# Performance work log

Measured on AMD Instinct MI355X. Metric: run time of the kernel, lower is better.

The kernel has to match this reference:

```python
import jax, jax.numpy as jnp
import numpy as np

NUM_GROUPS = 32
EPS = 1e-5


def group_norm(x, scale, bias):
    # x: [B, C, H, W]
    B, C, H, W = x.shape
    g = x.reshape(B, NUM_GROUPS, C // NUM_GROUPS * H * W)
    mean = g.mean(axis=-1, keepdims=True)
    var = g.var(axis=-1, keepdims=True)
    g = (g - mean) * jax.lax.rsqrt(var + EPS)
    g = g.reshape(B, C, H, W)
    return g * scale[None, :, None, None] + bias[None, :, None, None]


def conv1x1(x, w, b):
    # x: [B, C, H, W], w: [O, C], b: [O]
    return jnp.einsum('bchw,oc->bohw', x, w) + b[None, :, None, None]


def setup_inputs() -> dict:
    key = jax.random.key(0)
    ks = jax.random.split(key, 11)
    B, C, H, W = 32, 256, 32, 32
    s = 1.0 / np.sqrt(C)
    return {
        'x': jax.random.normal(ks[0], (B, C, H, W), jnp.float32),
        'gn_scale': jnp.ones((C,), jnp.float32),
        'gn_bias': jnp.zeros((C,), jnp.float32),
        'wq': jax.random.normal(ks[1], (C, C), jnp.float32) * s,
        'bq': jnp.zeros((C,), jnp.float32),
        'wk': jax.random.normal(ks[2], (C, C), jnp.float32) * s,
        'bk': jnp.zeros((C,), jnp.float32),
        'wv': jax.random.normal(ks[3], (C, C), jnp.float32) * s,
        'bv': jnp.zeros((C,), jnp.float32),
        'wo': jax.random.normal(ks[4], (C, C), jnp.float32) * s,
        'bo': jnp.zeros((C,), jnp.float32),
    }


def reference(x, gn_scale, gn_bias, wq, bq, wk, bk, wv, bv, wo, bo):
    B, C, H, W = x.shape
    h = group_norm(x, gn_scale, gn_bias)
    q = conv1x1(h, wq, bq).reshape(B, C, H * W)  # [B, C, N]
    k = conv1x1(h, wk, bk).reshape(B, C, H * W)
    v = conv1x1(h, wv, bv).reshape(B, C, H * W)
    # scores: [B, N, N]
    w = jnp.einsum('bcn,bcm->bnm', q, k) * (C ** -0.5)
    w = jax.nn.softmax(w, axis=-1)
    o = jnp.einsum('bnm,bcm->bcn', w, v).reshape(B, C, H, W)
    o = conv1x1(o, wo, bo)
    return x + o
```

## Files before the change

### kernel.cpp

```cpp
#include <hip/hip_runtime.h>

typedef __attribute__((ext_vector_type(4))) float f32x4;
typedef __attribute__((ext_vector_type(8))) short bf16x8;

__device__ __forceinline__ unsigned short f2bf(float f) {
  union { float f; unsigned u; } v; v.f = f;
  unsigned r = (v.u + 0x7FFFu + ((v.u >> 16) & 1u)) >> 16;
  return (unsigned short)r;
}

__device__ __forceinline__ unsigned cvt_pk_bf16(float lo, float hi) {
  unsigned r;
  asm("v_cvt_pk_bf16_f32 %0, %1, %2" : "=v"(r) : "v"(lo), "v"(hi));
  return r;
}

__device__ __forceinline__ void load16_lds(const void* g, void* l) {
  __builtin_amdgcn_global_load_lds(
      (__attribute__((address_space(1))) void*)(uintptr_t)g,
      (__attribute__((address_space(3))) void*)(unsigned int)(uintptr_t)l,
      16, 0, 0);
}

__global__ __launch_bounds__(256) void convert_w(
    const float* __restrict__ wq, const float* __restrict__ wk,
    const float* __restrict__ wv, const float* __restrict__ wo,
    const float* __restrict__ bq, const float* __restrict__ bk,
    unsigned short* __restrict__ wqkb, unsigned short* __restrict__ wvb,
    unsigned short* __restrict__ wob, float* __restrict__ bqkf) {
  const float* src[4] = {wq, wk, wv, wo};
  unsigned short* dst[4] = {wqkb, wqkb + 65536, wvb, wob};
  int ti = blockIdx.y;
  int idx = blockIdx.x * 256 + threadIdx.x;
  float4 v = ((const float4*)src[ti])[idx];
  ushort4 r;
  r.x = f2bf(v.x); r.y = f2bf(v.y); r.z = f2bf(v.z); r.w = f2bf(v.w);
  ((ushort4*)dst[ti])[idx] = r;
  if (ti == 3 && blockIdx.x == 0) {
    bqkf[threadIdx.x] = bq[threadIdx.x];
    bqkf[256 + threadIdx.x] = bk[threadIdx.x];
  }
}

__global__ __launch_bounds__(256) void gn_kernel(
    const float* __restrict__ x, const float* __restrict__ gamma,
    const float* __restrict__ beta, unsigned short* __restrict__ h) {
  __shared__ float xs[8 * 1024];
  __shared__ float red[16];
  const int t = threadIdx.x;
  const int b = blockIdx.x >> 5, g = blockIdx.x & 31;
  const float* xp = x + (size_t)(b * 256 + g * 8) * 1024;
  float s = 0.f, ss = 0.f;
#pragma unroll
  for (int j = 0; j < 8; ++j) {
    float4 v = ((const float4*)xp)[j * 256 + t];
    ((float4*)xs)[j * 256 + t] = v;
    s += v.x + v.y + v.z + v.w;
    ss += v.x * v.x + v.y * v.y + v.z * v.z + v.w * v.w;
  }
#pragma unroll
  for (int o = 32; o >= 1; o >>= 1) {
    s += __shfl_xor(s, o);
    ss += __shfl_xor(ss, o);
  }
  const int wave = t >> 6, lane = t & 63;
  if (lane == 0) { red[wave] = s; red[wave + 4] = ss; }
  __syncthreads();
  s = red[0] + red[1] + red[2] + red[3];
  ss = red[4] + red[5] + red[6] + red[7];
  float mean = s * (1.f / 8192.f);
  float var = ss * (1.f / 8192.f) - mean * mean;
  float rstd = rsqrtf(var + 1e-5f);
  float a[8], c[8];
#pragma unroll
  for (int ci = 0; ci < 8; ++ci) {
    float gm = gamma[g * 8 + ci], bt = beta[g * 8 + ci];
    a[ci] = rstd * gm;
    c[ci] = bt - mean * rstd * gm;
  }
  unsigned short* hb = h + (size_t)b * 1024 * 256 + g * 8;
#pragma unroll
  for (int j = 0; j < 4; ++j) {
    int n = j * 256 + t;
    float f0 = xs[0 * 1024 + n] * a[0] + c[0];
    float f1 = xs[1 * 1024 + n] * a[1] + c[1];
    float f2 = xs[2 * 1024 + n] * a[2] + c[2];
    float f3 = xs[3 * 1024 + n] * a[3] + c[3];
    float f4 = xs[4 * 1024 + n] * a[4] + c[4];
    float f5 = xs[5 * 1024 + n] * a[5] + c[5];
    float f6 = xs[6 * 1024 + n] * a[6] + c[6];
    float f7 = xs[7 * 1024 + n] * a[7] + c[7];
    uint4 o4;
    o4.x = (unsigned)f2bf(f0) | ((unsigned)f2bf(f1) << 16);
    o4.y = (unsigned)f2bf(f2) | ((unsigned)f2bf(f3) << 16);
    o4.z = (unsigned)f2bf(f4) | ((unsigned)f2bf(f5) << 16);
    o4.w = (unsigned)f2bf(f6) | ((unsigned)f2bf(f7) << 16);
    *(uint4*)(hb + (size_t)n * 256) = o4;
  }
}

template <bool OUT_F32, int BIAS_MODE, bool HAS_RES>
__global__ __launch_bounds__(256) void gemm_bt(
    const unsigned short* __restrict__ A, long long sAb,
    const unsigned short* __restrict__ Bm, long long sBb,
    void* __restrict__ Cv, long long sCb,
    const float* __restrict__ bias,
    const float* __restrict__ res, long long sRb,
    int M, int N, int K, float alpha) {
  __shared__ unsigned short As[128 * 32];
  __shared__ unsigned short Bs[128 * 32];
  const int t = threadIdx.x;
  const int wave = t >> 6, lane = t & 63;
  const int bm = blockIdx.y * 128, bn = blockIdx.x * 128;
  const int bz = blockIdx.z;
  const unsigned short* Ab = A + (size_t)bz * sAb;
  const unsigned short* Bb = Bm + (size_t)bz * sBb;
  const int wm = (wave >> 1) * 64, wn = (wave & 1) * 64;
  const int srow = t >> 2;
  const int schunk = t & 3;
  const int lrow = lane & 15, kg = lane >> 4;

  f32x4 acc[4][4] = {};

  for (int k0 = 0; k0 < K; k0 += 32) {
#pragma unroll
    for (int r = 0; r < 2; ++r) {
      int row = r * 64 + srow;
      int cs = schunk ^ ((row >> 1) & 3);
      const unsigned short* ga = Ab + (size_t)(bm + row) * K + (k0 + cs * 8);
      const unsigned short* gb = Bb + (size_t)(bn + row) * K + (k0 + cs * 8);
      load16_lds(ga, &As[(r * 64 + wave * 16) * 32]);
      load16_lds(gb, &Bs[(r * 64 + wave * 16) * 32]);
    }
    __syncthreads();
    bf16x8 af[4], bfr[4];
#pragma unroll
    for (int i = 0; i < 4; ++i) {
      int ra = wm + i * 16 + lrow;
      af[i] = *(const bf16x8*)&As[ra * 32 + ((kg ^ ((ra >> 1) & 3)) * 8)];
      int rb = wn + i * 16 + lrow;
      bfr[i] = *(const bf16x8*)&Bs[rb * 32 + ((kg ^ ((rb >> 1) & 3)) * 8)];
    }
#pragma unroll
    for (int i = 0; i < 4; ++i)
#pragma unroll
      for (int j = 0; j < 4; ++j)
        acc[i][j] = __builtin_amdgcn_mfma_f32_16x16x32_bf16(af[i], bfr[j], acc[i][j], 0, 0, 0);
    __syncthreads();
  }

#pragma unroll
  for (int i = 0; i < 4; ++i) {
#pragma unroll
    for (int j = 0; j < 4; ++j) {
#pragma unroll
      for (int r = 0; r < 4; ++r) {
        int m = bm + wm + i * 16 + (lane >> 4) * 4 + r;
        int n = bn + wn + j * 16 + lrow;
        float v = acc[i][j][r] * alpha;
        if constexpr (BIAS_MODE == 1) v += bias[m];
        if constexpr (BIAS_MODE == 2) v += bias[n];
        if constexpr (HAS_RES) v += res[(size_t)bz * sRb + (size_t)m * N + n];
        if constexpr (OUT_F32)
          ((float*)Cv)[(size_t)bz * sCb + (size_t)m * N + n] = v;
        else
          ((unsigned short*)Cv)[(size_t)bz * sCb + (size_t)m * N + n] = f2bf(v);
      }
    }
  }
}

__global__ __launch_bounds__(512, 2) void flash_attn(
    const unsigned short* __restrict__ qk,
    const unsigned short* __restrict__ vt,
    unsigned short* __restrict__ ot) {
  __shared__ unsigned short SMEM[81920];
  const int VS = 32768, PB = 65536;

  const int t = threadIdx.x;
  const int wave = t >> 6, lane = t & 63;
  const int wr = wave >> 1, wc = wave & 1;
  const int lrow = lane & 15, hi = lane >> 4;

  const int lbid = blockIdx.x;
  const int logical = (lbid & 7) * 32 + (lbid >> 3);
  const int b = logical >> 3;
  const int q0 = (logical & 7) * 128;

  const unsigned short* qb = qk + (size_t)b * 1024 * 512;
  const unsigned short* kb = qb + 256;
  const unsigned short* vb = vt + (size_t)b * 1024 * 256;

#pragma unroll
  for (int p = 0; p < 4; ++p) {
    int row = p * 16 + wave * 2 + (lane >> 5);
    int ch = (lane & 31) ^ (row & 31);
    load16_lds(kb + (size_t)row * 512 + ch * 8, &SMEM[(p * 16 + wave * 2) * 256]);
  }

  bf16x8 aq[2][8];
#pragma unroll
  for (int i = 0; i < 2; ++i)
#pragma unroll
    for (int kk = 0; kk < 8; ++kk)
      aq[i][kk] = *(const bf16x8*)(qb + (size_t)(q0 + wr * 32 + i * 16 + lrow) * 512 + kk * 32 + hi * 8);

  f32x4 acco[2][8] = {};
  float lsumP[2][4] = {{0.f, 0.f, 0.f, 0.f}, {0.f, 0.f, 0.f, 0.f}};

  asm volatile("s_waitcnt vmcnt(0)" ::: "memory");
  __builtin_amdgcn_s_barrier();
  __builtin_amdgcn_sched_barrier(0);

  const float SC2 = 0.0625f * 1.44269504f;

  for (int tt = 0; tt <= 16; ++tt) {
    const int cur = tt & 1, nxt = cur ^ 1;

    if (tt < 15) {
      const unsigned short* kn = kb + (size_t)(tt + 1) * 64 * 512;
#pragma unroll
      for (int p = 0; p < 4; ++p) {
        int row = p * 16 + wave * 2 + (lane >> 5);
        int ch = (lane & 31) ^ (row & 31);
        load16_lds(kn + (size_t)row * 512 + ch * 8, &SMEM[nxt * 16384 + (p * 16 + wave * 2) * 256]);
      }
    }
    if (tt < 16) {
      const unsigned short* vn = vb + tt * 64;
#pragma unroll
      for (int p = 0; p < 4; ++p) {
        int row = p * 64 + wave * 8 + (lane >> 3);
        int ch = (lane & 7) ^ (row & 7);
        load16_lds(vn + (size_t)row * 1024 + ch * 8, &SMEM[VS + cur * 16384 + (p * 64 + wave * 8) * 64]);
      }
    }

    f32x4 accs[2][2] = {};
    if (tt < 16) {
      const unsigned short* Kp = &SMEM[cur * 16384];
      __builtin_amdgcn_s_setprio(1);
#pragma unroll
      for (int kk = 0; kk < 8; ++kk) {
#pragma unroll
        for (int j = 0; j < 2; ++j) {
          int m = wc * 32 + j * 16 + lrow;
          bf16x8 bk8 = *(const bf16x8*)&Kp[m * 256 + (((kk * 4 + hi) ^ (m & 31)) * 8)];
          accs[0][j] = __builtin_amdgcn_mfma_f32_16x16x32_bf16(aq[0][kk], bk8, accs[0][j], 0, 0, 0);
          accs[1][j] = __builtin_amdgcn_mfma_f32_16x16x32_bf16(aq[1][kk], bk8, accs[1][j], 0, 0, 0);
        }
      }
      __builtin_amdgcn_s_setprio(0);
    }

    if (tt >= 1) {
      const unsigned short* Pp = &SMEM[PB + nxt * 8192];
      const unsigned short* Vp = &SMEM[VS + nxt * 16384];
#pragma unroll
      for (int kk2 = 0; kk2 < 2; ++kk2) {
        int qa0 = wr * 32 + lrow;
        int qa1 = qa0 + 16;
        bf16x8 pa0 = *(const bf16x8*)&Pp[qa0 * 64 + ((kk2 * 32 + hi * 8) ^ ((qa0 & 7) << 3))];
        bf16x8 pa1 = *(const bf16x8*)&Pp[qa1 * 64 + ((kk2 * 32 + hi * 8) ^ ((qa1 & 7) << 3))];
        __builtin_amdgcn_s_setprio(1);
#pragma unroll
        for (int jj = 0; jj < 8; ++jj) {
          int c = wc * 128 + jj * 16 + lrow;
          bf16x8 bv8 = *(const bf16x8*)&Vp[c * 64 + (((kk2 * 4 + hi) ^ (c & 7)) * 8)];
          acco[0][jj] = __builtin_amdgcn_mfma_f32_16x16x32_bf16(pa0, bv8, acco[0][jj], 0, 0, 0);
          acco[1][jj] = __builtin_amdgcn_mfma_f32_16x16x32_bf16(pa1, bv8, acco[1][jj], 0, 0, 0);
        }
        __builtin_amdgcn_s_setprio(0);
      }
    }

    if (tt < 16) {
      unsigned short* Pw = &SMEM[PB + cur * 8192];
#pragma unroll
      for (int i = 0; i < 2; ++i) {
        int qb4 = wr * 32 + i * 16 + hi * 4;
#pragma unroll
        for (int j = 0; j < 2; ++j) {
          int kvs = wc * 32 + j * 16 + lrow;
          float e0 = exp2f(accs[i][j][0] * SC2);
          float e1 = exp2f(accs[i][j][1] * SC2);
          float e2 = exp2f(accs[i][j][2] * SC2);
          float e3 = exp2f(accs[i][j][3] * SC2);
          lsumP[i][0] += e0; lsumP[i][1] += e1;
          lsumP[i][2] += e2; lsumP[i][3] += e3;
          unsigned p01 = cvt_pk_bf16(e0, e1);
          unsigned p23 = cvt_pk_bf16(e2, e3);
          Pw[(qb4 + 0) * 64 + (kvs ^ (((qb4 + 0) & 7) << 3))] = (unsigned short)p01;
          Pw[(qb4 + 1) * 64 + (kvs ^ (((qb4 + 1) & 7) << 3))] = (unsigned short)(p01 >> 16);
          Pw[(qb4 + 2) * 64 + (kvs ^ (((qb4 + 2) & 7) << 3))] = (unsigned short)p23;
          Pw[(qb4 + 3) * 64 + (kvs ^ (((qb4 + 3) & 7) << 3))] = (unsigned short)(p23 >> 16);
        }
      }
    }

    asm volatile("s_waitcnt vmcnt(0) lgkmcnt(0)" ::: "memory");
    __builtin_amdgcn_s_barrier();
    __builtin_amdgcn_sched_barrier(0);
  }

#pragma unroll
  for (int off = 1; off <= 8; off <<= 1)
#pragma unroll
    for (int i = 0; i < 2; ++i)
#pragma unroll
      for (int r = 0; r < 4; ++r)
        lsumP[i][r] += __shfl_xor(lsumP[i][r], off);
  float* red = (float*)SMEM;
  if (lrow == 0) {
#pragma unroll
    for (int i = 0; i < 2; ++i)
#pragma unroll
      for (int r = 0; r < 4; ++r)
        red[wc * 128 + wr * 32 + i * 16 + hi * 4 + r] = lsumP[i][r];
  }
  __syncthreads();

  unsigned short* ob = ot + (size_t)b * 1024 * 256;
#pragma unroll
  for (int i = 0; i < 2; ++i) {
    float inv[4];
#pragma unroll
    for (int r = 0; r < 4; ++r) {
      int rl = wr * 32 + i * 16 + hi * 4 + r;
      inv[r] = 1.f / (red[rl] + red[128 + rl]);
    }
#pragma unroll
    for (int jj = 0; jj < 8; ++jj)
#pragma unroll
      for (int r = 0; r < 4; ++r) {
        int n = q0 + wr * 32 + i * 16 + hi * 4 + r;
        int c = wc * 128 + jj * 16 + lrow;
        ob[(size_t)n * 256 + c] = f2bf(acco[i][jj][r] * inv[r]);
      }
  }
}

extern "C" void kernel_launch(void* const* d_in, const int* in_sizes, int n_in,
                              void* d_out, int out_size, void* d_ws, size_t ws_size,
                              hipStream_t stream) {
  const float* x    = (const float*)d_in[0];
  const float* gnsc = (const float*)d_in[1];
  const float* gnb  = (const float*)d_in[2];
  const float* wq   = (const float*)d_in[3];
  const float* bq   = (const float*)d_in[4];
  const float* wk   = (const float*)d_in[5];
  const float* bk   = (const float*)d_in[6];
  const float* wv   = (const float*)d_in[7];
  const float* bv   = (const float*)d_in[8];
  const float* wo   = (const float*)d_in[9];
  const float* bo   = (const float*)d_in[10];
  float* out = (float*)d_out;

  unsigned short* wqkb = (unsigned short*)d_ws;
  unsigned short* wvb  = wqkb + 131072;
  unsigned short* wob  = wvb + 65536;
  float*          bqkf = (float*)(wob + 65536);
  unsigned short* h    = wob + 65536 + 2048;
  unsigned short* qkb  = h + 8388608;
  unsigned short* vt   = qkb + 16777216;
  unsigned short* ot   = h;

  const long long sHN = 1024LL * 256;
  const long long sQK = 1024LL * 512;

  convert_w<<<dim3(64, 4), 256, 0, stream>>>(wq, wk, wv, wo, bq, bk, wqkb, wvb, wob, bqkf);
  gn_kernel<<<dim3(1024), 256, 0, stream>>>(x, gnsc, gnb, h);
  gemm_bt<false, 2, false><<<dim3(4, 8, 32), 256, 0, stream>>>(
      h, sHN, wqkb, 0, qkb, sQK, bqkf, nullptr, 0, 1024, 512, 256, 1.f);
  gemm_bt<false, 1, false><<<dim3(8, 2, 32), 256, 0, stream>>>(
      wvb, 0, h, sHN, vt, sHN, bv, nullptr, 0, 256, 1024, 256, 1.f);
  flash_attn<<<dim3(256), 512, 0, stream>>>(qkb, vt, ot);
  gemm_bt<true, 1, true><<<dim3(8, 2, 32), 256, 0, stream>>>(
      wob, 0, ot, sHN, out, sHN, bo, x, sHN, 256, 1024, 256, 1.f);
}
```

Baseline: 123.7 us.

## Use 32x32x16 MFMA for QK scores with transposed layout and folded scale

Replaces the 16x16x32 MFMA tiling of the Q·K^T score computation with a single 32x32x16 MFMA accumulator per wave, computing S^T (K as A operand, Q as B operand). Each lane then holds one query row's contiguous keys, so P can be written to LDS as 8-byte vector stores and the row-sum needs only one cross-lane shuffle. The softmax scale times log2(e) is folded into the bf16 Wq and bq during weight conversion, and the raw exp2 intrinsic is used. This removes per-element scaling, scalar LDS stores and shuffle reductions, but changes rounding of Q slightly and reshapes register usage.

```diff
diff --git a/kernel.cpp b/kernel.cpp
--- a/kernel.cpp
+++ b/kernel.cpp
@@ -1,6 +1,7 @@
 #include <hip/hip_runtime.h>
 
 typedef __attribute__((ext_vector_type(4))) float f32x4;
+typedef __attribute__((ext_vector_type(16))) float f32x16;
 typedef __attribute__((ext_vector_type(8))) short bf16x8;
 
 __device__ __forceinline__ unsigned short f2bf(float f) {
@@ -21,6 +22,8 @@
       (__attribute__((address_space(3))) void*)(unsigned int)(uintptr_t)l,
       16, 0, 0);
 }
+
+#define QSCALE 0.09016844f
 
 __global__ __launch_bounds__(256) void convert_w(
     const float* __restrict__ wq, const float* __restrict__ wk,
@@ -31,13 +34,15 @@
   const float* src[4] = {wq, wk, wv, wo};
   unsigned short* dst[4] = {wqkb, wqkb + 65536, wvb, wob};
   int ti = blockIdx.y;
+  float sc = (ti == 0) ? QSCALE : 1.f;
   int idx = blockIdx.x * 256 + threadIdx.x;
   float4 v = ((const float4*)src[ti])[idx];
   ushort4 r;
-  r.x = f2bf(v.x); r.y = f2bf(v.y); r.z = f2bf(v.z); r.w = f2bf(v.w);
+  r.x = f2bf(v.x * sc); r.y = f2bf(v.y * sc);
+  r.z = f2bf(v.z * sc); r.w = f2bf(v.w * sc);
   ((ushort4*)dst[ti])[idx] = r;
   if (ti == 3 && blockIdx.x == 0) {
-    bqkf[threadIdx.x] = bq[threadIdx.x];
+    bqkf[threadIdx.x] = bq[threadIdx.x] * QSCALE;
     bqkf[256 + threadIdx.x] = bk[threadIdx.x];
   }
 }
@@ -179,8 +184,9 @@
 
   const int t = threadIdx.x;
   const int wave = t >> 6, lane = t & 63;
-  const int wr = wave >> 1, wc = wave & 1;
+  const int wr = wave >> 1, wh = wave & 1;
   const int lrow = lane & 15, hi = lane >> 4;
+  const int l31 = lane & 31, h2 = lane >> 5;
 
   const int lbid = blockIdx.x;
   const int logical = (lbid & 7) * 32 + (lbid >> 3);
@@ -194,26 +200,22 @@
 #pragma unroll
   for (int p = 0; p < 4; ++p) {
     int row = p * 16 + wave * 2 + (lane >> 5);
-    int ch = (lane & 31) ^ (row & 31);
+    int ch = l31 ^ (row & 31);
     load16_lds(kb + (size_t)row * 512 + ch * 8, &SMEM[(p * 16 + wave * 2) * 256]);
   }
 
-  bf16x8 aq[2][8];
-#pragma unroll
-  for (int i = 0; i < 2; ++i)
-#pragma unroll
-    for (int kk = 0; kk < 8; ++kk)
-      aq[i][kk] = *(const bf16x8*)(qb + (size_t)(q0 + wr * 32 + i * 16 + lrow) * 512 + kk * 32 + hi * 8);
+  bf16x8 aq[16];
+#pragma unroll
+  for (int kk = 0; kk < 16; ++kk)
+    aq[kk] = *(const bf16x8*)(qb + (size_t)(q0 + wr * 32 + l31) * 512 + kk * 16 + h2 * 8);
 
   f32x4 acco[2][8] = {};
-  float lsumP[2][4] = {{0.f, 0.f, 0.f, 0.f}, {0.f, 0.f, 0.f, 0.f}};
+  float lsum = 0.f;
 
   asm volatile("s_waitcnt vmcnt(0)" ::: "memory");
   __builtin_amdgcn_s_barrier();
   __builtin_amdgcn_sched_barrier(0);
 
-  const float SC2 = 0.0625f * 1.44269504f;
-
   for (int tt = 0; tt <= 16; ++tt) {
     const int cur = tt & 1, nxt = cur ^ 1;
 
@@ -222,7 +224,7 @@
 #pragma unroll
       for (int p = 0; p < 4; ++p) {
         int row = p * 16 + wave * 2 + (lane >> 5);
-        int ch = (lane & 31) ^ (row & 31);
+        int ch = l31 ^ (row & 31);
         load16_lds(kn + (size_t)row * 512 + ch * 8, &SMEM[nxt * 16384 + (p * 16 + wave * 2) * 256]);
       }
     }
@@ -236,19 +238,15 @@
       }
     }
 
-    f32x4 accs[2][2] = {};
+    f32x16 accs = {};
     if (tt < 16) {
-      const unsigned short* Kp = &SMEM[cur * 16384];
+      const int kbase = cur * 16384;
+      const int krow = (wh * 32 + l31) * 256;
       __builtin_amdgcn_s_setprio(1);
 #pragma unroll
-      for (int kk = 0; kk < 8; ++kk) {
-#pragma unroll
-        for (int j = 0; j < 2; ++j) {
-          int m = wc * 32 + j * 16 + lrow;
-          bf16x8 bk8 = *(const bf16x8*)&Kp[m * 256 + (((kk * 4 + hi) ^ (m & 31)) * 8)];
-          accs[0][j] = __builtin_amdgcn_mfma_f32_16x16x32_bf16(aq[0][kk], bk8, accs[0][j], 0, 0, 0);
-          accs[1][j] = __builtin_amdgcn_mfma_f32_16x16x32_bf16(aq[1][kk], bk8, accs[1][j], 0, 0, 0);
-        }
+      for (int kk = 0; kk < 16; ++kk) {
+        bf16x8 kf = *(const bf16x8*)&SMEM[kbase + krow + (((kk * 2 + h2) ^ l31) << 3)];
+        accs = __builtin_amdgcn_mfma_f32_32x32x16_bf16(kf, aq[kk], accs, 0, 0, 0);
       }
       __builtin_amdgcn_s_setprio(0);
     }
@@ -265,7 +263,7 @@
         __builtin_amdgcn_s_setprio(1);
 #pragma unroll
         for (int jj = 0; jj < 8; ++jj) {
-          int c = wc * 128 + jj * 16 + lrow;
+          int c = wh * 128 + jj * 16 + lrow;
           bf16x8 bv8 = *(const bf16x8*)&Vp[c * 64 + (((kk2 * 4 + hi) ^ (c & 7)) * 8)];
           acco[0][jj] = __builtin_amdgcn_mfma_f32_16x16x32_bf16(pa0, bv8, acco[0][jj], 0, 0, 0);
           acco[1][jj] = __builtin_amdgcn_mfma_f32_16x16x32_bf16(pa1, bv8, acco[1][jj], 0, 0, 0);
@@ -275,26 +273,22 @@
     }
 
     if (tt < 16) {
-      unsigned short* Pw = &SMEM[PB + cur * 8192];
-#pragma unroll
-      for (int i = 0; i < 2; ++i) {
-        int qb4 = wr * 32 + i * 16 + hi * 4;
-#pragma unroll
-        for (int j = 0; j < 2; ++j) {
-          int kvs = wc * 32 + j * 16 + lrow;
-          float e0 = exp2f(accs[i][j][0] * SC2);
-          float e1 = exp2f(accs[i][j][1] * SC2);
-          float e2 = exp2f(accs[i][j][2] * SC2);
-          float e3 = exp2f(accs[i][j][3] * SC2);
-          lsumP[i][0] += e0; lsumP[i][1] += e1;
-          lsumP[i][2] += e2; lsumP[i][3] += e3;
-          unsigned p01 = cvt_pk_bf16(e0, e1);
-          unsigned p23 = cvt_pk_bf16(e2, e3);
-          Pw[(qb4 + 0) * 64 + (kvs ^ (((qb4 + 0) & 7) << 3))] = (unsigned short)p01;
-          Pw[(qb4 + 1) * 64 + (kvs ^ (((qb4 + 1) & 7) << 3))] = (unsigned short)(p01 >> 16);
-          Pw[(qb4 + 2) * 64 + (kvs ^ (((qb4 + 2) & 7) << 3))] = (unsigned short)p23;
-          Pw[(qb4 + 3) * 64 + (kvs ^ (((qb4 + 3) & 7) << 3))] = (unsigned short)(p23 >> 16);
-        }
+      char* Pw = (char*)&SMEM[PB + cur * 8192];
+      const int q = wr * 32 + l31;
+      const int qoff = q * 128 + (h2 << 3);
+      const int qx = (q & 7);
+#pragma unroll
+      for (int m = 0; m < 4; ++m) {
+        float e0 = __builtin_amdgcn_exp2f(accs[4 * m + 0]);
+        float e1 = __builtin_amdgcn_exp2f(accs[4 * m + 1]);
+        float e2 = __builtin_amdgcn_exp2f(accs[4 * m + 2]);
+        float e3 = __builtin_amdgcn_exp2f(accs[4 * m + 3]);
+        lsum += (e0 + e1) + (e2 + e3);
+        uint2 w2;
+        w2.x = cvt_pk_bf16(e0, e1);
+        w2.y = cvt_pk_bf16(e2, e3);
+        int c = wh * 4 + m;
+        *(uint2*)(Pw + qoff + ((c ^ qx) << 4)) = w2;
       }
     }
 
@@ -303,21 +297,9 @@
     __builtin_amdgcn_sched_barrier(0);
   }
 
-#pragma unroll
-  for (int off = 1; off <= 8; off <<= 1)
-#pragma unroll
-    for (int i = 0; i < 2; ++i)
-#pragma unroll
-      for (int r = 0; r < 4; ++r)
-        lsumP[i][r] += __shfl_xor(lsumP[i][r], off);
-  float* red = (float*)SMEM;
-  if (lrow == 0) {
-#pragma unroll
-    for (int i = 0; i < 2; ++i)
-#pragma unroll
-      for (int r = 0; r < 4; ++r)
-        red[wc * 128 + wr * 32 + i * 16 + hi * 4 + r] = lsumP[i][r];
-  }
+  lsum += __shfl_xor(lsum, 32);
+  float* lred = (float*)SMEM;
+  if (lane < 32) lred[wave * 32 + lane] = lsum;
   __syncthreads();
 
   unsigned short* ob = ot + (size_t)b * 1024 * 256;
@@ -327,14 +309,14 @@
 #pragma unroll
     for (int r = 0; r < 4; ++r) {
       int rl = wr * 32 + i * 16 + hi * 4 + r;
-      inv[r] = 1.f / (red[rl] + red[128 + rl]);
+      inv[r] = 1.f / (lred[wr * 64 + (rl & 31)] + lred[wr * 64 + 32 + (rl & 31)]);
     }
 #pragma unroll
     for (int jj = 0; jj < 8; ++jj)
 #pragma unroll
       for (int r = 0; r < 4; ++r) {
         int n = q0 + wr * 32 + i * 16 + hi * 4 + r;
-        int c = wc * 128 + jj * 16 + lrow;
+        int c = wh * 128 + jj * 16 + lrow;
         ob[(size_t)n * 256 + c] = f2bf(acco[i][jj][r] * inv[r]);
       }
   }
```

Result: faster. 118.7 us (-4.0%).
